# Optimization experiments

Measured on AMD Instinct MI355X. Metric: run time of the kernel, lower is better.

The kernel has to match this reference:

```python
import jax, jax.numpy as jnp
import numpy as np
from jax import lax

NUM_HEADS = 8
KERNEL_SIZE = 7
PADDING_L = 3
EPS = 1e-12


def pow2_quantize(w):
    # LinearShift: weights constrained to sign * 2^round(log2|w|) (bit-shift arithmetic),
    # with straight-through estimator for gradients.
    wq = jnp.sign(w) * jnp.exp2(jnp.round(jnp.log2(jnp.abs(w) + EPS)))
    return w + lax.stop_gradient(wq - w)


def setup_inputs() -> dict:
    key = jax.random.key(0)
    k1, k2, k3 = jax.random.split(key, 3)
    T, B, C = 4096, 16, 512
    x = jax.random.normal(k1, (T, B, C), dtype=jnp.float32)
    shift_W = jax.random.normal(k2, (C, C), dtype=jnp.float32) * (1.0 / np.sqrt(C))
    shift_b = jnp.zeros((C,), dtype=jnp.float32)
    # xavier-uniform-ish init for the light-conv weight (H, K)
    lim = np.sqrt(6.0 / (NUM_HEADS + KERNEL_SIZE))
    weight = jax.random.uniform(k3, (NUM_HEADS, KERNEL_SIZE), minval=-lim, maxval=lim, dtype=jnp.float32)
    return {"x": x, "shift_W": shift_W, "shift_b": shift_b, "weight": weight}


def reference(x, shift_W, shift_b, weight):
    T, B, C = x.shape
    H, K = weight.shape
    R = C // H
    # 1) shift-linear: power-of-two quantized weights, y = x @ Wq^T + b  (T,B,C)
    Wq = pow2_quantize(shift_W)
    y = jnp.einsum("tbc,dc->tbd", x, Wq) + shift_b
    # 2) light (depthwise, head-shared) convolution along time
    xc = jnp.transpose(y, (1, 2, 0))  # (B, C, T)
    w = jax.nn.softmax(weight, axis=-1)  # weight_softmax=True
    # expand head kernels to per-channel depthwise kernels: (C, 1, K)
    w_full = jnp.repeat(w, R, axis=0)[:, None, :]
    out = lax.conv_general_dilated(
        xc, w_full,
        window_strides=(1,),
        padding=[(PADDING_L, K - 1 - PADDING_L)],
        dimension_numbers=("NCH", "OIH", "NCH"),
        feature_group_count=C,
    )  # (B, C, T)
    return jnp.transpose(out, (2, 0, 1))  # (T, B, C)
```

## Files before the change

### kernel.cpp

```cpp
#include <hip/hip_runtime.h>

constexpr int T_DIM = 4096;
constexpr int B_DIM = 16;
constexpr int C_DIM = 512;
constexpr int K_CONV = 7;
constexpr int M_DIM = T_DIM * B_DIM;
constexpr int BC = B_DIM * C_DIM;

typedef __attribute__((ext_vector_type(8))) short bf16x8;
typedef __attribute__((ext_vector_type(4))) float f32x4;
typedef __attribute__((ext_vector_type(8))) float f32x8;
typedef __attribute__((ext_vector_type(4))) unsigned int u32x4;

__device__ __forceinline__ unsigned short f2bf(float f) {
  unsigned u = __float_as_uint(f);
  u += 0x7fffu + ((u >> 16) & 1u);
  return (unsigned short)(u >> 16);
}
__device__ __forceinline__ unsigned pack2(float a, float b) {
  return (unsigned)f2bf(a) | (((unsigned)f2bf(b)) << 16);
}
__device__ __forceinline__ u32x4 pack8(f32x4 lo, f32x4 hi) {
  u32x4 o;
  o[0] = pack2(lo[0], lo[1]);
  o[1] = pack2(lo[2], lo[3]);
  o[2] = pack2(hi[0], hi[1]);
  o[3] = pack2(hi[2], hi[3]);
  return o;
}

__global__ __launch_bounds__(256) void quantize_w(
    const float* __restrict__ W, unsigned short* __restrict__ Wq) {
  int i = blockIdx.x * 256 + threadIdx.x;
  float w = W[i];
  float a = fabsf(w) + 1e-12f;
  float q = exp2f(rintf(log2f(a)));
  q = (w > 0.f) ? q : ((w < 0.f) ? -q : 0.f);
  Wq[i] = f2bf(q);
}

constexpr int BK = 32;

__global__ __launch_bounds__(256, 2) void gemm_bt(
    const float* __restrict__ X, const short* __restrict__ Bt,
    const float* __restrict__ bias, unsigned short* __restrict__ Y) {
  constexpr int K = C_DIM, N = C_DIM;
  __shared__ __align__(16) short As[128 * BK];
  __shared__ __align__(16) short Bs[128 * BK];

  const int t    = threadIdx.x;
  const int lane = t & 63;
  const int wid  = t >> 6;
  const int m0 = blockIdx.y * 128;
  const int n0 = blockIdx.x * 128;

  const int sr = t >> 2;
  const int sc = (t & 3) * 8;
  const float* pX0 = X + (long)(m0 + sr) * K + sc;
  const float* pX1 = X + (long)(m0 + 64 + sr) * K + sc;
  const short* pB0 = Bt + (long)(n0 + sr) * K + sc;
  const short* pB1 = Bt + (long)(n0 + 64 + sr) * K + sc;

  const int fr = lane & 15;
  const int fq = lane >> 4;
  const int wm = (wid >> 1) * 64;
  const int wn = (wid & 1) * 64;

  f32x4 acc[4][4] = {};

  for (int k0 = 0; k0 < K; k0 += BK) {
    f32x4 xa0 = *(const f32x4*)(pX0 + k0);
    f32x4 xa1 = *(const f32x4*)(pX0 + k0 + 4);
    f32x4 xb0 = *(const f32x4*)(pX1 + k0);
    f32x4 xb1 = *(const f32x4*)(pX1 + k0 + 4);
    bf16x8 b0 = *(const bf16x8*)(pB0 + k0);
    bf16x8 b1 = *(const bf16x8*)(pB1 + k0);
    u32x4 a0 = pack8(xa0, xa1);
    u32x4 a1 = pack8(xb0, xb1);
    __syncthreads();
    *(u32x4*)&As[sr * BK + sc]         = a0;
    *(u32x4*)&As[(64 + sr) * BK + sc]  = a1;
    *(bf16x8*)&Bs[sr * BK + sc]        = b0;
    *(bf16x8*)&Bs[(64 + sr) * BK + sc] = b1;
    __syncthreads();

    bf16x8 af[4], bfr[4];
#pragma unroll
    for (int i = 0; i < 4; ++i)
      af[i] = *(const bf16x8*)&As[(wm + i * 16 + fr) * BK + fq * 8];
#pragma unroll
    for (int j = 0; j < 4; ++j)
      bfr[j] = *(const bf16x8*)&Bs[(wn + j * 16 + fr) * BK + fq * 8];
#pragma unroll
    for (int i = 0; i < 4; ++i)
#pragma unroll
      for (int j = 0; j < 4; ++j)
        acc[i][j] = __builtin_amdgcn_mfma_f32_16x16x32_bf16(af[i], bfr[j], acc[i][j], 0, 0, 0);
  }

#pragma unroll
  for (int j = 0; j < 4; ++j) {
    const int gn = n0 + wn + j * 16 + fr;
    const float bv = bias[gn];
#pragma unroll
    for (int i = 0; i < 4; ++i) {
#pragma unroll
      for (int r = 0; r < 4; ++r) {
        const int gm = m0 + wm + i * 16 + fq * 4 + r;
        Y[(long)gm * N + gn] = f2bf(acc[i][j][r] + bv);
      }
    }
  }
}

constexpr int CHT = 16;

__device__ __forceinline__ u32x4 loadY(const unsigned short* Y, int t, long off) {
  if ((unsigned)t < (unsigned)T_DIM)
    return *(const u32x4*)(Y + (long)t * BC + off);
  u32x4 z = {0u, 0u, 0u, 0u};
  return z;
}

__device__ __forceinline__ f32x8 unpack8(u32x4 u) {
  f32x8 r;
#pragma unroll
  for (int i = 0; i < 4; ++i) {
    unsigned w = u[i];
    r[2 * i]     = __uint_as_float(w << 16);
    r[2 * i + 1] = __uint_as_float(w & 0xffff0000u);
  }
  return r;
}

__global__ __launch_bounds__(256) void lconv(
    const unsigned short* __restrict__ Y, const float* __restrict__ W,
    float* __restrict__ O) {
  const int tid  = blockIdx.x * 256 + threadIdx.x;
  const int cvec = tid & 63;
  const int b    = (tid >> 6) & 15;
  const int tc   = tid >> 10;
  const int t0   = tc * CHT;
  const long off = (long)b * C_DIM + cvec * 8;
  const int h    = cvec >> 3;

  float wf[K_CONV];
  float mx = -1e30f;
#pragma unroll
  for (int k = 0; k < K_CONV; ++k) { wf[k] = W[h * K_CONV + k]; mx = fmaxf(mx, wf[k]); }
  float s = 0.f;
#pragma unroll
  for (int k = 0; k < K_CONV; ++k) { wf[k] = __expf(wf[k] - mx); s += wf[k]; }
  const float inv = 1.f / s;
#pragma unroll
  for (int k = 0; k < K_CONV; ++k) wf[k] *= inv;

  f32x8 win[K_CONV];
#pragma unroll
  for (int i = 0; i < 6; ++i) win[i] = unpack8(loadY(Y, t0 - 3 + i, off));

#pragma unroll
  for (int j = 0; j < CHT; ++j) {
    win[6] = unpack8(loadY(Y, t0 + 3 + j, off));
    f32x8 acc = win[0] * wf[0];
#pragma unroll
    for (int k = 1; k < K_CONV; ++k) acc += win[k] * wf[k];
    float* op = O + (long)(t0 + j) * BC + off;
    *(f32x4*)op       = f32x4{acc[0], acc[1], acc[2], acc[3]};
    *(f32x4*)(op + 4) = f32x4{acc[4], acc[5], acc[6], acc[7]};
#pragma unroll
    for (int k = 0; k < 6; ++k) win[k] = win[k + 1];
  }
}

extern "C" void kernel_launch(void* const* d_in, const int* in_sizes, int n_in,
                              void* d_out, int out_size, void* d_ws, size_t ws_size,
                              hipStream_t stream) {
  const float* x       = (const float*)d_in[0];
  const float* shift_W = (const float*)d_in[1];
  const float* shift_b = (const float*)d_in[2];
  const float* weight  = (const float*)d_in[3];
  float* out = (float*)d_out;

  unsigned short* Wq = (unsigned short*)d_ws;
  unsigned short* Y  = Wq + C_DIM * C_DIM;

  quantize_w<<<(C_DIM * C_DIM) / 256, 256, 0, stream>>>(shift_W, Wq);
  gemm_bt<<<dim3(C_DIM / 128, M_DIM / 128), 256, 0, stream>>>(
      x, (const short*)Wq, shift_b, Y);
  lconv<<<(M_DIM / CHT) * (C_DIM / 8) / 256, 256, 0, stream>>>(Y, weight, out);
}
```

Baseline: 326.7 us.

## Pad GEMM LDS rows, prefetch next K tile, remap blocks per XCD, lengthen conv chunks

The GEMM now stores its LDS tiles with a padded row stride of 40 to reduce bank conflicts on the fragment reads. Global loads for the next K tile are issued right after the barrier, so they overlap the MFMA work on the current tile. The grid becomes 1D, and block IDs are remapped so each XCD handles a contiguous band of M rows, which improves L2 reuse of X and Wq. The light-conv time chunk doubles to 32, reducing redundant halo loads at the cost of fewer threads and more registers per thread.

New measurement: 320.7 us. Within noise of the previous version (-1.8%).

```diff
diff --git a/kernel.cpp b/kernel.cpp
--- a/kernel.cpp
+++ b/kernel.cpp
@@ -40,19 +40,26 @@
 }
 
 constexpr int BK = 32;
+constexpr int LDS_STRIDE = 40;
 
 __global__ __launch_bounds__(256, 2) void gemm_bt(
     const float* __restrict__ X, const short* __restrict__ Bt,
     const float* __restrict__ bias, unsigned short* __restrict__ Y) {
   constexpr int K = C_DIM, N = C_DIM;
-  __shared__ __align__(16) short As[128 * BK];
-  __shared__ __align__(16) short Bs[128 * BK];
+  __shared__ __align__(16) short As[128 * LDS_STRIDE];
+  __shared__ __align__(16) short Bs[128 * LDS_STRIDE];
+
+  const int id   = blockIdx.x;
+  const int xcd  = id & 7;
+  const int slot = id >> 3;
+  const int nb   = slot & 3;
+  const int mb   = xcd * 64 + (slot >> 2);
+  const int m0 = mb * 128;
+  const int n0 = nb * 128;
 
   const int t    = threadIdx.x;
   const int lane = t & 63;
   const int wid  = t >> 6;
-  const int m0 = blockIdx.y * 128;
-  const int n0 = blockIdx.x * 128;
 
   const int sr = t >> 2;
   const int sc = (t & 3) * 8;
@@ -68,29 +75,40 @@
 
   f32x4 acc[4][4] = {};
 
+  f32x4 xa0 = *(const f32x4*)(pX0);
+  f32x4 xa1 = *(const f32x4*)(pX0 + 4);
+  f32x4 xb0 = *(const f32x4*)(pX1);
+  f32x4 xb1 = *(const f32x4*)(pX1 + 4);
+  bf16x8 b0 = *(const bf16x8*)(pB0);
+  bf16x8 b1 = *(const bf16x8*)(pB1);
+
   for (int k0 = 0; k0 < K; k0 += BK) {
-    f32x4 xa0 = *(const f32x4*)(pX0 + k0);
-    f32x4 xa1 = *(const f32x4*)(pX0 + k0 + 4);
-    f32x4 xb0 = *(const f32x4*)(pX1 + k0);
-    f32x4 xb1 = *(const f32x4*)(pX1 + k0 + 4);
-    bf16x8 b0 = *(const bf16x8*)(pB0 + k0);
-    bf16x8 b1 = *(const bf16x8*)(pB1 + k0);
     u32x4 a0 = pack8(xa0, xa1);
     u32x4 a1 = pack8(xb0, xb1);
+    bf16x8 bs0 = b0, bs1 = b1;
     __syncthreads();
-    *(u32x4*)&As[sr * BK + sc]         = a0;
-    *(u32x4*)&As[(64 + sr) * BK + sc]  = a1;
-    *(bf16x8*)&Bs[sr * BK + sc]        = b0;
-    *(bf16x8*)&Bs[(64 + sr) * BK + sc] = b1;
+    *(u32x4*)&As[sr * LDS_STRIDE + sc]         = a0;
+    *(u32x4*)&As[(64 + sr) * LDS_STRIDE + sc]  = a1;
+    *(bf16x8*)&Bs[sr * LDS_STRIDE + sc]        = bs0;
+    *(bf16x8*)&Bs[(64 + sr) * LDS_STRIDE + sc] = bs1;
     __syncthreads();
 
+    if (k0 + BK < K) {
+      xa0 = *(const f32x4*)(pX0 + k0 + BK);
+      xa1 = *(const f32x4*)(pX0 + k0 + BK + 4);
+      xb0 = *(const f32x4*)(pX1 + k0 + BK);
+      xb1 = *(const f32x4*)(pX1 + k0 + BK + 4);
+      b0 = *(const bf16x8*)(pB0 + k0 + BK);
+      b1 = *(const bf16x8*)(pB1 + k0 + BK);
+    }
+
     bf16x8 af[4], bfr[4];
 #pragma unroll
     for (int i = 0; i < 4; ++i)
-      af[i] = *(const bf16x8*)&As[(wm + i * 16 + fr) * BK + fq * 8];
+      af[i] = *(const bf16x8*)&As[(wm + i * 16 + fr) * LDS_STRIDE + fq * 8];
 #pragma unroll
     for (int j = 0; j < 4; ++j)
-      bfr[j] = *(const bf16x8*)&Bs[(wn + j * 16 + fr) * BK + fq * 8];
+      bfr[j] = *(const bf16x8*)&Bs[(wn + j * 16 + fr) * LDS_STRIDE + fq * 8];
 #pragma unroll
     for (int i = 0; i < 4; ++i)
 #pragma unroll
@@ -113,7 +131,7 @@
   }
 }
 
-constexpr int CHT = 16;
+constexpr int CHT = 32;
 
 __device__ __forceinline__ u32x4 loadY(const unsigned short* Y, int t, long off) {
   if ((unsigned)t < (unsigned)T_DIM)
@@ -186,7 +204,7 @@
   unsigned short* Y  = Wq + C_DIM * C_DIM;
 
   quantize_w<<<(C_DIM * C_DIM) / 256, 256, 0, stream>>>(shift_W, Wq);
-  gemm_bt<<<dim3(C_DIM / 128, M_DIM / 128), 256, 0, stream>>>(
+  gemm_bt<<<(M_DIM / 128) * (C_DIM / 128), 256, 0, stream>>>(
       x, (const short*)Wq, shift_b, Y);
   lconv<<<(M_DIM / CHT) * (C_DIM / 8) / 256, 256, 0, stream>>>(Y, weight, out);
 }
```
